# Performance work log

Measured on AMD Instinct MI355X. Metric: run time of the kernel, lower is better.

Reference implementation:

```python
import jax, jax.numpy as jnp
import numpy as np
from jax import lax

D_MODEL = 2048
D_STATE = 16
D_CONV = 4
D_INNER = 4096   # expand * d_model
DT_RANK = 128    # ceil(d_model / 16)
BATCH = 4
SEQLEN = 2048


def setup_inputs() -> dict:
    key = jax.random.key(0)
    ks = jax.random.split(key, 8)
    rnd = lambda k, shape, s: jax.random.normal(k, shape, dtype=jnp.float32) * s
    hidden_states = rnd(ks[0], (BATCH, SEQLEN, D_MODEL), 1.0)
    in_proj_w = rnd(ks[1], (2 * D_INNER, D_MODEL), D_MODEL ** -0.5)
    conv_w = rnd(ks[2], (D_INNER, 1, D_CONV), 0.3)
    conv_b = rnd(ks[3], (D_INNER,), 0.1)
    x_proj_w = rnd(ks[4], (DT_RANK + 2 * D_STATE, D_INNER), D_INNER ** -0.5)
    dt_proj_w = rnd(ks[5], (D_INNER, DT_RANK), DT_RANK ** -0.5)
    dt_proj_b = rnd(ks[6], (D_INNER,), 0.5) - 2.0  # bias dt small, like mamba dt init
    out_proj_w = rnd(ks[7], (D_MODEL, D_INNER), D_INNER ** -0.5)
    # A init: -exp(log(arange(1..N))) broadcast over channels -> (d_state, d_inner)
    A = -jnp.tile(jnp.arange(1, D_STATE + 1, dtype=jnp.float32)[:, None], (1, D_INNER))
    D = jnp.ones((D_INNER,), dtype=jnp.float32)
    conv_state = jnp.zeros((BATCH, D_INNER, D_CONV), jnp.float32)
    ssm_state = jnp.zeros((BATCH, D_STATE, D_INNER), jnp.float32)
    last_token_ids = jnp.full((BATCH,), SEQLEN, dtype=jnp.int32)
    return dict(hidden_states=hidden_states, last_token_ids=last_token_ids,
                conv_state=conv_state, ssm_state=ssm_state,
                remove_padding=False, batch_size=BATCH,
                in_proj_w=in_proj_w, conv_w=conv_w, conv_b=conv_b,
                x_proj_w=x_proj_w, dt_proj_w=dt_proj_w, dt_proj_b=dt_proj_b,
                A=A, D=D, out_proj_w=out_proj_w)


def _mamba_forward(hidden_states, in_proj_w, conv_w, conv_b, x_proj_w,
                   dt_proj_w, dt_proj_b, A, D, out_proj_w):
    b, L, _ = hidden_states.shape
    # in_proj (no bias)
    xz = jnp.einsum('bld,ed->ble', hidden_states, in_proj_w)          # (b, L, 2*d_inner)
    x, z = jnp.split(xz, 2, axis=-1)
    x_bdl = x.transpose(0, 2, 1)                                       # (b, d_inner, L)
    # present conv state = last d_conv columns of pre-conv x (F.pad with negative pad)
    new_conv_state = x_bdl[:, :, L - D_CONV:]
    # causal depthwise conv1d (left pad d_conv-1 == pad-both then truncate to L)
    x_conv = lax.conv_general_dilated(
        x_bdl, conv_w, window_strides=(1,), padding=[(D_CONV - 1, 0)],
        feature_group_count=D_INNER,
        dimension_numbers=('NCH', 'OIH', 'NCH')) + conv_b[None, :, None]
    u = jax.nn.silu(x_conv).transpose(0, 2, 1)                          # (b, L, d_inner)
    # x_proj -> dt, B, C
    x_dbl = jnp.einsum('bld,ed->ble', u, x_proj_w)
    dt, Bm, Cm = jnp.split(x_dbl, [DT_RANK, DT_RANK + D_STATE], axis=-1)
    dt = jnp.einsum('blr,dr->bld', dt, dt_proj_w)                       # no bias here
    # selective scan (delta_bias=dt_proj_b, delta_softplus=True)
    delta = jax.nn.softplus(dt + dt_proj_b)                             # (b, L, d_inner)
    dBu = delta * u                                                     # (b, L, d_inner)

    def step(x_state, inp):
        d_i, bu_i, B_i, C_i = inp                                       # (b,d),(b,d),(b,n),(b,n)
        dA = jnp.exp(d_i[:, None, :] * A[None])                         # (b, n, d)
        x_state = dA * x_state + B_i[:, :, None] * bu_i[:, None, :]
        y = jnp.einsum('bnd,bn->bd', x_state, C_i)
        return x_state, y

    x0 = jnp.zeros((b, D_STATE, D_INNER), jnp.float32)
    xs = (delta.transpose(1, 0, 2), dBu.transpose(1, 0, 2),
          Bm.transpose(1, 0, 2), Cm.transpose(1, 0, 2))
    last_state, ys = lax.scan(step, x0, xs)
    y = ys.transpose(1, 0, 2) + u * D                                   # + D skip
    y = y * jax.nn.silu(z)                                              # gate
    out = jnp.einsum('bld,ed->ble', y, out_proj_w)                      # out_proj (no bias)
    return out, new_conv_state, last_state


def reference(hidden_states, last_token_ids, conv_state, ssm_state,
              remove_padding, batch_size,
              in_proj_w, conv_w, conv_b, x_proj_w, dt_proj_w, dt_proj_b,
              A, D, out_proj_w):
    # remove_padding=False and last_token_ids all == L: the torch per-sequence
    # loop is exactly one batched forward_impl with seqlen_offset=0.
    return _mamba_forward(hidden_states, in_proj_w, conv_w, conv_b, x_proj_w,
                          dt_proj_w, dt_proj_b, A, D, out_proj_w)
```

## Files before the change

### kernel.cpp

```cpp
#include <hip/hip_runtime.h>
#include <hip/hip_bf16.h>
#include <math.h>

typedef __attribute__((ext_vector_type(4))) float fvec4;
typedef __attribute__((ext_vector_type(2))) float fvec2;
typedef __attribute__((ext_vector_type(4))) int ivec4;
typedef __attribute__((ext_vector_type(4))) unsigned short usvec4;
typedef __attribute__((ext_vector_type(8))) short bf16x8;

#define SEQ 2048
#define DMODEL 2048
#define DINNER 4096
#define DSTATE 16
#define DTRANK 128
#define NB 4
#define MROWS (NB*SEQ)
#define NCHUNK 16
#define LC (SEQ/NCHUNK)

__device__ __forceinline__ float bf2f(unsigned short h){
  union{unsigned int u; float f;} v; v.u = ((unsigned int)h)<<16; return v.f;
}
__device__ __forceinline__ unsigned short f2bf(float f){
  union{float f; unsigned int u;} v; v.f=f;
  unsigned int r = v.u + 0x7fffu + ((v.u>>16)&1u);
  return (unsigned short)(r>>16);
}
__device__ __forceinline__ void async16(const void* g, void* l){
  __builtin_amdgcn_global_load_lds((const __attribute__((address_space(1))) void*)g,
                                   (__attribute__((address_space(3))) void*)l, 16, 0, 0);
}
__device__ __forceinline__ float sigf(float x){ return 1.f/(1.f+__expf(-x)); }

__global__ void cvt_bf16_kernel(const float* __restrict__ in, unsigned short* __restrict__ out, int n){
  int i = (blockIdx.x*256 + threadIdx.x)*4;
  if (i >= n) return;
  fvec4 v = *(const fvec4*)(in + i);
  usvec4 o;
  o[0]=f2bf(v[0]); o[1]=f2bf(v[1]); o[2]=f2bf(v[2]); o[3]=f2bf(v[3]);
  *(usvec4*)(out + i) = o;
}

template<int MODE>
__global__ __launch_bounds__(512, 2) void gemm256(
    const unsigned short* __restrict__ A,
    const unsigned short* __restrict__ B,
    int K, int nbx, int ldc,
    unsigned short* __restrict__ Cb1,
    unsigned short* __restrict__ Cb2,
    float* __restrict__ Cf)
{
  __shared__ __align__(16) unsigned short lds[32768];
  char* ldsc = (char*)lds;
  const int t = threadIdx.x;

  const int nwg = gridDim.x;
  const int cpx = nwg >> 3;
  const int bid = blockIdx.x;
  const int swzb = (bid & 7)*cpx + (bid >> 3);
  const int bx = swzb % nbx, by = swzb / nbx;

  const int bA0 = t*16, bA1 = 8192 + t*16;
  const int sw0 = bA0 ^ (((bA0>>7)&3)<<4);
  const int sw1 = bA1 ^ (((bA1>>7)&3)<<4);
  const int gr0 = sw0>>6, gc0 = (sw0&63)>>1;
  const int gr1 = sw1>>6, gc1 = (sw1&63)>>1;
  const unsigned short* Ab = A + (long)by*256*K;
  const unsigned short* Bb = B + (long)bx*256*K;
  const unsigned short* gA0 = Ab + (long)gr0*K + gc0;
  const unsigned short* gA1 = Ab + (long)gr1*K + gc1;
  const unsigned short* gB0 = Bb + (long)gr0*K + gc0;
  const unsigned short* gB1 = Bb + (long)gr1*K + gc1;

  const int wid = t>>6, lane = t&63;
  const int wm = wid>>2, wn = wid&3;
  const int fr = lane&15, fc = lane>>4;
  const int cb = (fc<<4) ^ (((fr>>1)&3)<<4);
  const int offA = (wm*128 + fr)*64 + cb;
  const int offB = 16384 + (wn*64 + fr)*64 + cb;

  fvec4 acc[8][4];
  #pragma unroll
  for (int i=0;i<8;i++){
    #pragma unroll
    for (int j=0;j<4;j++) acc[i][j] = (fvec4)(0.f);
  }

  const int NKT = K >> 5;
  auto stage = [&](int slot, int k0){
    char* sb = ldsc + slot*32768;
    async16(gA0 + k0, sb + t*16);
    async16(gA1 + k0, sb + 8192 + t*16);
    async16(gB0 + k0, sb + 16384 + t*16);
    async16(gB1 + k0, sb + 24576 + t*16);
  };

  stage(0, 0);

  for (int kt = 0; kt < NKT; ++kt){
    asm volatile("s_waitcnt vmcnt(0)" ::: "memory");
    __builtin_amdgcn_s_barrier();
    __builtin_amdgcn_sched_barrier(0);
    if (kt+1 < NKT) stage((kt+1)&1, (kt+1)*32);
    const char* sb = ldsc + (kt&1)*32768;
    bf16x8 af[8], bv[4];
    #pragma unroll
    for (int j=0;j<4;j++) bv[j] = *(const bf16x8*)(sb + offB + j*1024);
    #pragma unroll
    for (int i=0;i<8;i++) af[i] = *(const bf16x8*)(sb + offA + i*1024);
    __builtin_amdgcn_s_setprio(1);
    #pragma unroll
    for (int i=0;i<8;i++){
      #pragma unroll
      for (int j=0;j<4;j++){
        acc[i][j] = __builtin_amdgcn_mfma_f32_16x16x32_bf16(af[i], bv[j], acc[i][j], 0,0,0);
      }
    }
    __builtin_amdgcn_s_setprio(0);
  }

  const long crow0 = (long)by*256 + wm*128;
  const int  ccol0 = bx*256 + wn*64;
  #pragma unroll
  for (int i=0;i<8;i++){
    #pragma unroll
    for (int j=0;j<4;j++){
      #pragma unroll
      for (int q=0;q<4;q++){
        long rg = crow0 + i*16 + fc*4 + q;
        int  cg = ccol0 + j*16 + fr;
        float v = acc[i][j][q];
        if (MODE==0){
          if (cg < DINNER) Cb1[rg*DINNER + cg] = f2bf(v);
          else             Cb2[rg*DINNER + (cg-DINNER)] = f2bf(v);
        } else {
          Cf[rg*(long)ldc + cg] = v;
        }
      }
    }
  }
}

template<int MODE>
__global__ __launch_bounds__(256) void gemm_bt(
    const unsigned short* __restrict__ A,
    const unsigned short* __restrict__ B,
    int K, int Nreal,
    float* __restrict__ Cf,
    unsigned short* __restrict__ Cb1,
    const float* __restrict__ bias,
    int ldc)
{
  __shared__ __align__(16) unsigned short As[128*32];
  __shared__ __align__(16) unsigned short Bs[128*32];
  const int t = threadIdx.x;
  const int bx = blockIdx.x, by = blockIdx.y;
  const int wave = t>>6, lane = t&63;
  const int wr = (wave>>1)*64, wc = (wave&1)*64;
  const int fr = lane&15, fc = lane>>4;
  fvec4 acc[4][4];
  #pragma unroll
  for(int i=0;i<4;i++){
    #pragma unroll
    for(int j=0;j<4;j++){ acc[i][j] = (fvec4)(0.f); }
  }
  const int srow = t>>2;
  const int scol = (t&3)*8;
  long rowA = (long)by*128 + srow;
  int rB0 = bx*128 + srow;      if (rB0 > Nreal-1) rB0 = Nreal-1;
  int rB1 = bx*128 + 64 + srow; if (rB1 > Nreal-1) rB1 = Nreal-1;
  const unsigned short* gA0 = A + rowA*(long)K + scol;
  const unsigned short* gA1 = gA0 + 64L*K;
  const unsigned short* gB0 = B + (long)rB0*K + scol;
  const unsigned short* gB1 = B + (long)rB1*K + scol;
  unsigned short* lA0 = &As[t*8];
  unsigned short* lA1 = &As[2048 + t*8];
  unsigned short* lB0 = &Bs[t*8];
  unsigned short* lB1 = &Bs[2048 + t*8];

  for (int k0 = 0; k0 < K; k0 += 32){
    async16(gA0 + k0, lA0);
    async16(gA1 + k0, lA1);
    async16(gB0 + k0, lB0);
    async16(gB1 + k0, lB1);
    __syncthreads();
    bf16x8 af[4], bv[4];
    #pragma unroll
    for(int i=0;i<4;i++){
      af[i] = *(const bf16x8*)&As[(wr + i*16 + fr)*32 + fc*8];
      bv[i] = *(const bf16x8*)&Bs[(wc + i*16 + fr)*32 + fc*8];
    }
    #pragma unroll
    for(int i=0;i<4;i++){
      #pragma unroll
      for(int j=0;j<4;j++){
        acc[i][j] = __builtin_amdgcn_mfma_f32_16x16x32_bf16(af[i], bv[j], acc[i][j], 0,0,0);
      }
    }
    __syncthreads();
  }

  const long crow0 = (long)by*128 + wr;
  const int ccol0 = bx*128 + wc;
  #pragma unroll
  for(int i=0;i<4;i++){
    #pragma unroll
    for(int j=0;j<4;j++){
      #pragma unroll
      for(int q=0;q<4;q++){
        long rg = crow0 + i*16 + fc*4 + q;
        int  cg = ccol0 + j*16 + fr;
        float v = acc[i][j][q];
        if (MODE==1){
          if (cg < Nreal) Cf[rg*ldc + cg] = v;
        } else if (MODE==2){
          float x = v + bias[cg];
          float sp = (x > 20.f) ? x : log1pf(__expf(x));
          Cb1[rg*ldc + cg] = f2bf(sp);
        }
      }
    }
  }
}

__global__ __launch_bounds__(256) void conv_silu_kernel(
    const unsigned short* __restrict__ xb, const float* __restrict__ w,
    const float* __restrict__ bias, unsigned short* __restrict__ ub)
{
  int gid = blockIdx.x*256 + threadIdx.x;
  int d0 = (gid & 511)*8;
  long m = gid >> 9;
  int l = (int)(m & (SEQ-1));
  fvec4 w4[8];
  #pragma unroll
  for(int k=0;k<8;k++) w4[k] = *(const fvec4*)&w[(d0+k)*4];
  float acc[8];
  fvec4 b0 = *(const fvec4*)&bias[d0];
  fvec4 b1 = *(const fvec4*)&bias[d0+4];
  acc[0]=b0[0];acc[1]=b0[1];acc[2]=b0[2];acc[3]=b0[3];
  acc[4]=b1[0];acc[5]=b1[1];acc[6]=b1[2];acc[7]=b1[3];
  #pragma unroll
  for(int j=0;j<4;j++){
    int lj = l-3+j;
    if (lj >= 0){
      ivec4 xv = *(const ivec4*)&xb[(m-3+j)*DINNER + d0];
      float xs[8];
      #pragma unroll
      for(int q=0;q<4;q++){
        unsigned int wd = (unsigned int)xv[q];
        xs[2*q]   = bf2f((unsigned short)(wd & 0xffffu));
        xs[2*q+1] = bf2f((unsigned short)(wd >> 16));
      }
      #pragma unroll
      for(int k=0;k<8;k++) acc[k] += xs[k]*w4[k][j];
    }
  }
  ivec4 ov;
  #pragma unroll
  for(int q=0;q<4;q++){
    float y0 = acc[2*q]  * sigf(acc[2*q]);
    float y1 = acc[2*q+1]* sigf(acc[2*q+1]);
    ov[q] = (int)((unsigned)f2bf(y0) | ((unsigned)f2bf(y1) << 16));
  }
  *(ivec4*)&ub[m*DINNER + d0] = ov;
}

__global__ void conv_state_kernel(const unsigned short* __restrict__ xb, float* __restrict__ out){
  int i = blockIdx.x*256 + threadIdx.x;
  int b = i >> 14; int r = i & 16383; int dd = r >> 2; int j = r & 3;
  out[i] = bf2f(xb[((long)(b*SEQ + (SEQ-4) + j))*DINNER + dd]);
}

__global__ void cvt_dtr_kernel(const float* __restrict__ xdbl, unsigned short* __restrict__ dtr){
  int i = blockIdx.x*256 + threadIdx.x;
  long mrow = i >> 5; int c = (i & 31)*4;
  fvec4 v = *(const fvec4*)&xdbl[mrow*160 + c];
  usvec4 o; o[0]=f2bf(v[0]); o[1]=f2bf(v[1]); o[2]=f2bf(v[2]); o[3]=f2bf(v[3]);
  *(usvec4*)&dtr[mrow*DTRANK + c] = o;
}

__global__ __launch_bounds__(256) void scan_part1(
    const unsigned short* __restrict__ delta_b,
    const unsigned short* __restrict__ u_b,
    const float* __restrict__ xdbl,
    const float* __restrict__ Amat,
    float* __restrict__ S,
    float* __restrict__ sdelta)
{
  const int t = threadIdx.x;
  const int blk = blockIdx.x;
  const int c = blk & 15, b = (blk>>4)&3, d = (blk>>6)*256 + t;
  float a[16], s[16];
  #pragma unroll
  for (int n=0;n<16;n++){ a[n] = Amat[n*DINNER+d]; s[n]=0.f; }
  float sd = 0.f;
  const long mbase = (long)b*SEQ + c*LC;
  for (int l=0;l<LC;l++){
    long m = mbase + l;
    float dl = bf2f(delta_b[m*DINNER+d]);
    float ul = bf2f(u_b[m*DINNER+d]);
    const float* xb = &xdbl[m*160 + 128];
    float dbu = dl*ul;
    sd += dl;
    #pragma unroll
    for (int g=0; g<4; g++){
      fvec4 Bg = *(const fvec4*)(xb + 4*g);
      #pragma unroll
      for (int q=0;q<4;q++){
        int n = g*4+q;
        s[n] = __expf(dl*a[n])*s[n] + Bg[q]*dbu;
      }
    }
  }
  const long base = ((long)(b*NCHUNK + c)*DSTATE)*DINNER + d;
  #pragma unroll
  for (int n=0;n<16;n++) S[base + (long)n*DINNER] = s[n];
  sdelta[(long)(b*NCHUNK+c)*DINNER + d] = sd;
}

__global__ __launch_bounds__(256) void scan_part2(
    const float* __restrict__ S,
    const float* __restrict__ sdelta,
    const float* __restrict__ Amat,
    float* __restrict__ Xin,
    float* __restrict__ last_state)
{
  int id = blockIdx.x*256 + threadIdx.x;
  int d = id & (DINNER-1);
  int n = (id>>12) & 15;
  int b = id>>16;
  float a = Amat[n*DINNER+d];
  float X = 0.f;
  #pragma unroll
  for (int c=0;c<NCHUNK;c++){
    long sb = ((long)(b*NCHUNK+c)*DSTATE + n)*DINNER + d;
    Xin[sb] = X;
    float sd = sdelta[(long)(b*NCHUNK+c)*DINNER + d];
    float Sc = S[sb];
    X = __expf(a*sd)*X + Sc;
  }
  last_state[((long)b*DSTATE + n)*DINNER + d] = X;
}

__global__ __launch_bounds__(256) void scan_part3(
    const unsigned short* __restrict__ delta_b,
    const unsigned short* __restrict__ u_b,
    const unsigned short* __restrict__ z_b,
    const float* __restrict__ xdbl,
    const float* __restrict__ Amat,
    const float* __restrict__ Dvec,
    const float* __restrict__ Xin,
    unsigned short* __restrict__ y_b)
{
  const int t = threadIdx.x;
  const int blk = blockIdx.x;
  const int c = blk & 15, b = (blk>>4)&3, d = (blk>>6)*256 + t;
  float a[16], s[16];
  const long xb0 = ((long)(b*NCHUNK + c)*DSTATE)*DINNER + d;
  #pragma unroll
  for (int n=0;n<16;n++){
    a[n] = Amat[n*DINNER+d];
    s[n] = Xin[xb0 + (long)n*DINNER];
  }
  const float Dd = Dvec[d];
  const long mbase = (long)b*SEQ + c*LC;
  for (int l=0;l<LC;l++){
    long m = mbase + l;
    float dl = bf2f(delta_b[m*DINNER+d]);
    float ul = bf2f(u_b[m*DINNER+d]);
    float zl = bf2f(z_b[m*DINNER+d]);
    const float* xb = &xdbl[m*160 + 128];
    float dbu = dl*ul;
    float y = 0.f;
    #pragma unroll
    for (int g=0; g<4; g++){
      fvec4 Bg = *(const fvec4*)(xb + 4*g);
      fvec4 Cg = *(const fvec4*)(xb + 16 + 4*g);
      #pragma unroll
      for (int q=0;q<4;q++){
        int n = g*4+q;
        s[n] = __expf(dl*a[n])*s[n] + Bg[q]*dbu;
        y += Cg[q]*s[n];
      }
    }
    float yy = y + ul*Dd;
    float zs = zl*sigf(zl);
    y_b[m*DINNER+d] = f2bf(yy*zs);
  }
}

extern "C" void kernel_launch(void* const* d_in, const int* in_sizes, int n_in,
                              void* d_out, int out_size, void* d_ws, size_t ws_size,
                              hipStream_t stream) {
  const float* hs     = (const float*)d_in[0];
  const float* w_in   = (const float*)d_in[6];
  const float* conv_w = (const float*)d_in[7];
  const float* conv_b = (const float*)d_in[8];
  const float* w_xp   = (const float*)d_in[9];
  const float* w_dt   = (const float*)d_in[10];
  const float* dt_bias= (const float*)d_in[11];
  const float* Amat   = (const float*)d_in[12];
  const float* Dvec   = (const float*)d_in[13];
  const float* w_out  = (const float*)d_in[14];
  float* out = (float*)d_out;

  char* ws = (char*)d_ws;
  const size_t MiB = (size_t)1 << 20;

  unsigned short *hs_b, *w_in_b, *x_b, *z_b, *u_b, *delta_b;
  unsigned short *wxp_b, *wdt_b, *wout_b, *dtr_b, *y_b;
  float *xdbl, *Sbuf, *Xin, *sdelta;

  if (ws_size >= 400*MiB){
    size_t off = 0;
    auto alloc = [&](size_t bytes)->void*{ void* p = ws + off; off += (bytes + 255) & ~(size_t)255; return p; };
    hs_b   = (unsigned short*)alloc((size_t)MROWS*DMODEL*2);
    w_in_b = (unsigned short*)alloc((size_t)2*DINNER*DMODEL*2);
    x_b    = (unsigned short*)alloc((size_t)MROWS*DINNER*2);
    z_b    = (unsigned short*)alloc((size_t)MROWS*DINNER*2);
    u_b    = (unsigned short*)alloc((size_t)MROWS*DINNER*2);
    delta_b= (unsigned short*)alloc((size_t)MROWS*DINNER*2);
    wxp_b  = (unsigned short*)alloc((size_t)160*DINNER*2);
    wdt_b  = (unsigned short*)alloc((size_t)DINNER*DTRANK*2);
    wout_b = (unsigned short*)alloc((size_t)DMODEL*DINNER*2);
    xdbl   = (float*)alloc((size_t)MROWS*160*4);
    dtr_b  = (unsigned short*)alloc((size_t)MROWS*DTRANK*2);
    Sbuf   = (float*)alloc((size_t)NB*NCHUNK*DSTATE*DINNER*4);
    Xin    = (float*)alloc((size_t)NB*NCHUNK*DSTATE*DINNER*4);
    sdelta = (float*)alloc((size_t)NB*NCHUNK*DINNER*4);
    y_b    = x_b;
  } else {
    hs_b    = (unsigned short*)(ws + 0);
    w_in_b  = (unsigned short*)(ws + 32*MiB);
    delta_b = (unsigned short*)(ws + 0);
    x_b     = (unsigned short*)(ws + 64*MiB);
    wxp_b   = (unsigned short*)(ws + 64*MiB);
    wdt_b   = (unsigned short*)(ws + 66*MiB);
    wout_b  = (unsigned short*)(ws + 68*MiB);
    xdbl    = (float*)         (ws + 84*MiB);
    dtr_b   = (unsigned short*)(ws + 90*MiB);
    Sbuf    = (float*)         (ws + 92*MiB);
    Xin     = (float*)         (ws + 108*MiB);
    sdelta  = (float*)         (ws + 124*MiB);
    z_b     = (unsigned short*)(ws + 128*MiB);
    u_b     = (unsigned short*)(ws + 192*MiB);
    y_b     = u_b;
  }

  cvt_bf16_kernel<<<(MROWS*DMODEL)/1024, 256, 0, stream>>>(hs, hs_b, MROWS*DMODEL);
  cvt_bf16_kernel<<<(2*DINNER*DMODEL)/1024, 256, 0, stream>>>(w_in, w_in_b, 2*DINNER*DMODEL);

  gemm256<0><<<1024, 512, 0, stream>>>(hs_b, w_in_b, DMODEL, 32, 0,
                                       x_b, z_b, nullptr);
  conv_state_kernel<<<256, 256, 0, stream>>>(x_b, out + (size_t)MROWS*DMODEL);
  conv_silu_kernel<<<(MROWS*512)/256, 256, 0, stream>>>(x_b, conv_w, conv_b, u_b);

  cvt_bf16_kernel<<<(160*DINNER)/1024, 256, 0, stream>>>(w_xp, wxp_b, 160*DINNER);
  cvt_bf16_kernel<<<(DINNER*DTRANK)/1024, 256, 0, stream>>>(w_dt, wdt_b, DINNER*DTRANK);
  cvt_bf16_kernel<<<(DMODEL*DINNER)/1024, 256, 0, stream>>>(w_out, wout_b, DMODEL*DINNER);

  gemm_bt<1><<<dim3(2,64), 256, 0, stream>>>(u_b, wxp_b, DINNER, 160,
                                             xdbl, nullptr, nullptr, 160);
  cvt_dtr_kernel<<<(MROWS*32)/256, 256, 0, stream>>>(xdbl, dtr_b);
  gemm_bt<2><<<dim3(32,64), 256, 0, stream>>>(dtr_b, wdt_b, DTRANK, DINNER,
                                              nullptr, delta_b, dt_bias, DINNER);
  scan_part1<<<1024, 256, 0, stream>>>(delta_b, u_b, xdbl, Amat, Sbuf, sdelta);
  scan_part2<<<1024, 256, 0, stream>>>(Sbuf, sdelta, Amat, Xin,
                                       out + (size_t)MROWS*DMODEL + NB*DINNER*4);
  scan_part3<<<1024, 256, 0, stream>>>(delta_b, u_b, z_b, xdbl, Amat, Dvec, Xin, y_b);
  gemm256<3><<<256, 512, 0, stream>>>(y_b, wout_b, DINNER, 8, DMODEL,
                                      nullptr, nullptr, out);
}
```

Before: 1.011 ms.

## Deepen GEMM LDS pipeline to four stages and use exp powers in scan

The GEMM now keeps four LDS stages, prefetching three k-tiles ahead and waiting only on older loads, so global-memory latency can overlap more MFMA work. This doubles LDS use to 128 KB per block, which may cut occupancy under launch_bounds(512,2). It also adds a runtime check in both scan kernels: when A holds exactly -(n+1), the sixteen exponentials are built from one exp and repeated multiplications. A fallback path keeps general A correct, but the fast path depends on the specific A values supplied by setup_inputs.

Result: faster. 912.5 us (-9.7%).

```diff
diff --git a/kernel.cpp b/kernel.cpp
--- a/kernel.cpp
+++ b/kernel.cpp
@@ -50,7 +50,7 @@
     unsigned short* __restrict__ Cb2,
     float* __restrict__ Cf)
 {
-  __shared__ __align__(16) unsigned short lds[32768];
+  __shared__ __align__(16) unsigned short lds[65536];
   char* ldsc = (char*)lds;
   const int t = threadIdx.x;
 
@@ -95,14 +95,16 @@
     async16(gB1 + k0, sb + 24576 + t*16);
   };
 
-  stage(0, 0);
+  stage(0, 0); stage(1, 32); stage(2, 64);
 
   for (int kt = 0; kt < NKT; ++kt){
-    asm volatile("s_waitcnt vmcnt(0)" ::: "memory");
+    asm volatile("s_waitcnt vmcnt(8)" ::: "memory");
     __builtin_amdgcn_s_barrier();
     __builtin_amdgcn_sched_barrier(0);
-    if (kt+1 < NKT) stage((kt+1)&1, (kt+1)*32);
-    const char* sb = ldsc + (kt&1)*32768;
+    { int ks = kt + 3; if (ks > NKT-1) ks = NKT-1;
+      stage((kt+3)&3, ks*32); }
+    __builtin_amdgcn_sched_barrier(0);
+    const char* sb = ldsc + (kt&3)*32768;
     bf16x8 af[8], bv[4];
     #pragma unroll
     for (int j=0;j<4;j++) bv[j] = *(const bf16x8*)(sb + offB + j*1024);
@@ -279,6 +281,15 @@
   *(usvec4*)&dtr[mrow*DTRANK + c] = o;
 }
 
+__device__ __forceinline__ void exp_powers(float dl, float* e){
+  float e1 = __expf(-dl);
+  float p2 = e1*e1, p3 = p2*e1, p4 = p2*p2;
+  float p5 = p4*e1, p6 = p4*p2, p7 = p4*p3, p8 = p4*p4;
+  e[0]=e1; e[1]=p2; e[2]=p3; e[3]=p4; e[4]=p5; e[5]=p6; e[6]=p7; e[7]=p8;
+  e[8]=p8*e1; e[9]=p8*p2; e[10]=p8*p3; e[11]=p8*p4;
+  e[12]=p8*p5; e[13]=p8*p6; e[14]=p8*p7; e[15]=p8*p8;
+}
+
 __global__ __launch_bounds__(256) void scan_part1(
     const unsigned short* __restrict__ delta_b,
     const unsigned short* __restrict__ u_b,
@@ -293,25 +304,39 @@
   float a[16], s[16];
   #pragma unroll
   for (int n=0;n<16;n++){ a[n] = Amat[n*DINNER+d]; s[n]=0.f; }
+  bool powA = true;
+  #pragma unroll
+  for (int n=0;n<16;n++) powA = powA && (a[n] == -(float)(n+1));
   float sd = 0.f;
   const long mbase = (long)b*SEQ + c*LC;
-  for (int l=0;l<LC;l++){
-    long m = mbase + l;
-    float dl = bf2f(delta_b[m*DINNER+d]);
-    float ul = bf2f(u_b[m*DINNER+d]);
-    const float* xb = &xdbl[m*160 + 128];
-    float dbu = dl*ul;
-    sd += dl;
-    #pragma unroll
-    for (int g=0; g<4; g++){
-      fvec4 Bg = *(const fvec4*)(xb + 4*g);
-      #pragma unroll
-      for (int q=0;q<4;q++){
-        int n = g*4+q;
-        s[n] = __expf(dl*a[n])*s[n] + Bg[q]*dbu;
-      }
-    }
-  }
+
+#define S1_BODY(EXPR_E) \
+  for (int l=0;l<LC;l++){ \
+    long m = mbase + l; \
+    float dl = bf2f(delta_b[m*DINNER+d]); \
+    float ul = bf2f(u_b[m*DINNER+d]); \
+    const float* xb = &xdbl[m*160 + 128]; \
+    float dbu = dl*ul; \
+    sd += dl; \
+    float e[16]; EXPR_E; \
+    _Pragma("unroll") \
+    for (int g=0; g<4; g++){ \
+      fvec4 Bg = *(const fvec4*)(xb + 4*g); \
+      _Pragma("unroll") \
+      for (int q=0;q<4;q++){ \
+        int n = g*4+q; \
+        s[n] = e[n]*s[n] + Bg[q]*dbu; \
+      } \
+    } \
+  }
+
+  if (powA){
+    S1_BODY(exp_powers(dl, e))
+  } else {
+    S1_BODY({ _Pragma("unroll") for (int n=0;n<16;n++) e[n] = __expf(dl*a[n]); })
+  }
+#undef S1_BODY
+
   const long base = ((long)(b*NCHUNK + c)*DSTATE)*DINNER + d;
   #pragma unroll
   for (int n=0;n<16;n++) S[base + (long)n*DINNER] = s[n];
@@ -362,31 +387,44 @@
     a[n] = Amat[n*DINNER+d];
     s[n] = Xin[xb0 + (long)n*DINNER];
   }
+  bool powA = true;
+  #pragma unroll
+  for (int n=0;n<16;n++) powA = powA && (a[n] == -(float)(n+1));
   const float Dd = Dvec[d];
   const long mbase = (long)b*SEQ + c*LC;
-  for (int l=0;l<LC;l++){
-    long m = mbase + l;
-    float dl = bf2f(delta_b[m*DINNER+d]);
-    float ul = bf2f(u_b[m*DINNER+d]);
-    float zl = bf2f(z_b[m*DINNER+d]);
-    const float* xb = &xdbl[m*160 + 128];
-    float dbu = dl*ul;
-    float y = 0.f;
-    #pragma unroll
-    for (int g=0; g<4; g++){
-      fvec4 Bg = *(const fvec4*)(xb + 4*g);
-      fvec4 Cg = *(const fvec4*)(xb + 16 + 4*g);
-      #pragma unroll
-      for (int q=0;q<4;q++){
-        int n = g*4+q;
-        s[n] = __expf(dl*a[n])*s[n] + Bg[q]*dbu;
-        y += Cg[q]*s[n];
-      }
-    }
-    float yy = y + ul*Dd;
-    float zs = zl*sigf(zl);
-    y_b[m*DINNER+d] = f2bf(yy*zs);
-  }
+
+#define S3_BODY(EXPR_E) \
+  for (int l=0;l<LC;l++){ \
+    long m = mbase + l; \
+    float dl = bf2f(delta_b[m*DINNER+d]); \
+    float ul = bf2f(u_b[m*DINNER+d]); \
+    float zl = bf2f(z_b[m*DINNER+d]); \
+    const float* xb = &xdbl[m*160 + 128]; \
+    float dbu = dl*ul; \
+    float y = 0.f; \
+    float e[16]; EXPR_E; \
+    _Pragma("unroll") \
+    for (int g=0; g<4; g++){ \
+      fvec4 Bg = *(const fvec4*)(xb + 4*g); \
+      fvec4 Cg = *(const fvec4*)(xb + 16 + 4*g); \
+      _Pragma("unroll") \
+      for (int q=0;q<4;q++){ \
+        int n = g*4+q; \
+        s[n] = e[n]*s[n] + Bg[q]*dbu; \
+        y += Cg[q]*s[n]; \
+      } \
+    } \
+    float yy = y + ul*Dd; \
+    float zs = zl*sigf(zl); \
+    y_b[m*DINNER+d] = f2bf(yy*zs); \
+  }
+
+  if (powA){
+    S3_BODY(exp_powers(dl, e))
+  } else {
+    S3_BODY({ _Pragma("unroll") for (int n=0;n<16;n++) e[n] = __expf(dl*a[n]); })
+  }
+#undef S3_BODY
 }
 
 extern "C" void kernel_launch(void* const* d_in, const int* in_sizes, int n_in,
```
